# Kernel optimization log

Measured on AMD Instinct MI355X. Metric: run time of the kernel, lower is better.

Reference implementation:

```python
import jax, jax.numpy as jnp
import numpy as np

CODEBOOK_SIZE = 8192
CODEBOOK_DIM = 16
IN_DIM = 512


def setup_inputs() -> dict:
    key = jax.random.key(0)
    k1, k2, k3 = jax.random.split(key, 3)
    input_values = jax.random.normal(k1, (8, 4096, IN_DIM), dtype=jnp.float32)
    # xavier_uniform for Linear(IN_DIM -> CODEBOOK_DIM), weight shape (out, in) in torch
    limit = float(np.sqrt(6.0 / (IN_DIM + CODEBOOK_DIM)))
    proj_weight = jax.random.uniform(k2, (CODEBOOK_DIM, IN_DIM), dtype=jnp.float32, minval=-limit, maxval=limit)
    code_book = jax.random.normal(k3, (CODEBOOK_SIZE, CODEBOOK_DIM), dtype=jnp.float32)
    return {"input_values": input_values, "proj_weight": proj_weight, "code_book": code_book}


def reference(input_values, proj_weight, code_book):
    # targets: (B, L, d) = input @ W^T  (bias-free random projection)
    targets = jnp.einsum("bld,cd->blc", input_values, proj_weight)  # (B, L, 16)
    # Squared L2 distance via expansion ||t - c||^2 = ||t||^2 - 2 t.c + ||c||^2.
    # argmin is identical to argmin of the norm; avoids the (B,L,K,d) broadcast tensor.
    t_sq = jnp.sum(targets * targets, axis=-1, keepdims=True)        # (B, L, 1)
    c_sq = jnp.sum(code_book * code_book, axis=-1)                   # (K,)
    cross = jnp.einsum("blc,kc->blk", targets, code_book)            # (B, L, K)
    dist_sq = t_sq - 2.0 * cross + c_sq                              # (B, L, K)
    labels = jnp.argmin(dist_sq, axis=-1)                            # (B, L) int
    return labels
```

## Files before the change

kernel.cpp:

```cpp
#include <hip/hip_runtime.h>
#include <stdint.h>

#define IN_DIM 512
#define CB 8192
#define CD 16
#define NROWS 32768
#define DELTAQ 8e-3f
#define FMAXV 3.402823466e38f

typedef short bf16x8 __attribute__((ext_vector_type(8)));
typedef float f32x4 __attribute__((ext_vector_type(4)));

__device__ inline unsigned short f2bf(float x) {
    unsigned u = __float_as_uint(x);
    unsigned r = u + 0x7FFFu + ((u >> 16) & 1u);
    return (unsigned short)(r >> 16);
}
__device__ inline float bf2f(unsigned short h) { return __uint_as_float(((unsigned)h) << 16); }
__device__ inline unsigned umin32(unsigned a, unsigned b) { return a < b ? a : b; }
__device__ inline unsigned umax32(unsigned a, unsigned b) { return a > b ? a : b; }
__device__ inline unsigned long long shfl_xor_u64(unsigned long long x, int m) {
    double d = __shfl_xor(__longlong_as_double((long long)x), m, 64);
    return (unsigned long long)__double_as_longlong(d);
}

__global__ __launch_bounds__(256) void prep_kernel(const float* __restrict__ cb,
                                                   float* __restrict__ csq,
                                                   float* __restrict__ csqoff,
                                                   bf16x8* __restrict__ Bp,
                                                   int* __restrict__ counter) {
    int id = blockIdx.x * 256 + threadIdx.x;
    if (id == 0) counter[0] = 0;
    if (id < CB) {
        const float4* p = (const float4*)(cb + (size_t)id * CD);
        float s = 0.f;
#pragma unroll
        for (int j = 0; j < 4; ++j) {
            float4 v = p[j];
            s += v.x * v.x + v.y * v.y + v.z * v.z + v.w * v.w;
        }
        csq[id] = s;
        csqoff[id] = s + 256.0f;
    }
    int slot = id & 63;
    int nt = id >> 6;
    int q = slot >> 4;
    int n = nt * 16 + (slot & 15);
    int d0 = (q & 1) * 8;
    bool lo = (q < 2);
    const float* src = cb + (size_t)n * CD + d0;
    bf16x8 v;
#pragma unroll
    for (int j = 0; j < 8; ++j) {
        float x = src[j];
        unsigned short a = f2bf(x);
        unsigned short b = f2bf(x - bf2f(a));
        v[j] = (short)(lo ? a : b);
    }
    Bp[id] = v;
}

__global__ __launch_bounds__(256) void proj_partial_kernel(const float* __restrict__ in,
                                                           const float* __restrict__ W,
                                                           float* __restrict__ partials) {
    __shared__ float4 LIN[2048];
    __shared__ float4 WL[16 * 33];
    int tid = threadIdx.x;
    int lane = tid & 63;
    int dg = __builtin_amdgcn_readfirstlane(tid >> 6);
    int strip = blockIdx.x >> 2;
    int c = blockIdx.x & 3;
    int rowbase = strip * 64;
    const float4* inp4 = (const float4*)in;
    const float4* W4 = (const float4*)W;

#pragma unroll
    for (int u = 0; u < 2; ++u) {
        int f = tid + u * 256;
        int d = f >> 5, o = f & 31;
        WL[d * 33 + o] = W4[(size_t)d * 128 + c * 32 + o];
    }
#pragma unroll
    for (int u = 0; u < 8; ++u) {
        int f = tid + u * 256;
        int o = f & 31, r = f >> 5;
        LIN[o * 64 + (r ^ (o & 7))] = inp4[(size_t)(rowbase + r) * 128 + c * 32 + o];
    }
    __syncthreads();

    float acc[4];
#pragma unroll
    for (int i = 0; i < 4; ++i) acc[i] = 0.f;
#pragma unroll 4
    for (int j = 0; j < 32; ++j) {
        float4 v = LIN[j * 64 + (lane ^ (j & 7))];
#pragma unroll
        for (int i = 0; i < 4; ++i) {
            float4 w = WL[(4 * dg + i) * 33 + j];
            acc[i] += v.x * w.x + v.y * w.y + v.z * w.z + v.w * w.w;
        }
    }
    float* o = partials + (size_t)c * NROWS * CD + (size_t)(rowbase + lane) * CD + 4 * dg;
#pragma unroll
    for (int i = 0; i < 4; ++i) o[i] = acc[i];
}

__global__ __launch_bounds__(256) void proj_combine_kernel(const float* __restrict__ partials,
                                                           float* __restrict__ tprime) {
    int idx = blockIdx.x * 256 + threadIdx.x;
    const size_t P = (size_t)NROWS * CD;
    float p0 = partials[idx];
    float p1 = partials[P + idx];
    float p2 = partials[2 * P + idx];
    float p3 = partials[3 * P + idx];
    tprime[idx] = -2.f * (((p0 + p1) + p2) + p3);
}

__global__ __launch_bounds__(512, 6) void scan_kernel(
        const float* __restrict__ tprime, const float* __restrict__ csqoff,
        const bf16x8* __restrict__ Bp, int* __restrict__ out,
        int* __restrict__ queue, int* __restrict__ counter) {
    __shared__ float tbuf[32][17];
    __shared__ unsigned long long m_k[32][8];
    __shared__ unsigned m_s2[32][8];

    int tid = threadIdx.x;
    int lane = tid & 63;
    int e = __builtin_amdgcn_readfirstlane(tid >> 6);
    int rowbase = blockIdx.x * 32;

    tbuf[tid >> 4][tid & 15] = tprime[(size_t)rowbase * CD + tid];
    __syncthreads();

    int q = lane >> 4;
    int col = lane & 15;
    int d0 = (q & 1) * 8;
    bool lo = (q < 2);

    bf16x8 A1[2], A2[2];
#pragma unroll
    for (int g = 0; g < 2; ++g) {
        int arow = 16 * g + col;
#pragma unroll
        for (int j = 0; j < 8; ++j) {
            float x = tbuf[arow][d0 + j];
            unsigned short t1 = f2bf(x);
            unsigned short t2 = f2bf(x - bf2f(t1));
            A1[g][j] = (short)t1;
            A2[g][j] = (short)(lo ? t2 : 0);
        }
    }

    unsigned s1[2][4], s2[2][4];
#pragma unroll
    for (int g = 0; g < 2; ++g)
#pragma unroll
        for (int r = 0; r < 4; ++r) { s1[g][r] = 0xFFFFFFFFu; s2[g][r] = 0xFFFFFFFFu; }

    int nt0 = e * 64;
    const bf16x8* pb = Bp + (size_t)nt0 * 64 + lane;
    const float* csqp = csqoff + nt0 * 16 + col;

#pragma unroll 4
    for (int t = 0; t < 64; ++t) {
        bf16x8 b = pb[(size_t)t * 64];
        float cs = csqp[t * 16];
        f32x4 ini = {cs, cs, cs, cs};
        unsigned tt = (unsigned)t;
#pragma unroll
        for (int g = 0; g < 2; ++g) {
            f32x4 acc = __builtin_amdgcn_mfma_f32_16x16x32_bf16(A1[g], b, ini, 0, 0, 0);
            acc = __builtin_amdgcn_mfma_f32_16x16x32_bf16(A2[g], b, acc, 0, 0, 0);
#pragma unroll
            for (int r = 0; r < 4; ++r) {
                unsigned k = (__float_as_uint(acc[r]) & 0xFFFFFFC0u) | tt;
                s2[g][r] = umin32(s2[g][r], umax32(k, s1[g][r]));
                s1[g][r] = umin32(s1[g][r], k);
            }
        }
    }

#pragma unroll
    for (int g = 0; g < 2; ++g)
#pragma unroll
        for (int r = 0; r < 4; ++r) {
            unsigned long long FK = ((unsigned long long)(s1[g][r] & 0xFFFFFFC0u) << 13)
                                  | ((unsigned long long)e << 10)
                                  | ((unsigned long long)(s1[g][r] & 63u) << 4)
                                  | (unsigned long long)col;
            unsigned s2q = s2[g][r] & 0xFFFFFFC0u;
#pragma unroll
            for (int m = 1; m < 16; m <<= 1) {
                unsigned long long oFK = shfl_xor_u64(FK, m);
                unsigned os2 = (unsigned)__shfl_xor((int)s2q, m, 64);
                unsigned qa = (unsigned)(FK >> 13);
                unsigned qb = (unsigned)(oFK >> 13);
                s2q = umin32(umin32(s2q, os2), umax32(qa, qb));
                FK = oFK < FK ? oFK : FK;
            }
            if (col == 0) {
                int rl = 16 * g + 4 * q + r;
                m_k[rl][e] = FK;
                m_s2[rl][e] = s2q;
            }
        }
    __syncthreads();

    if (tid < 32) {
        unsigned long long mFK = m_k[tid][0];
        unsigned g1 = (unsigned)(m_k[tid][0] >> 13);
        unsigned g2 = m_s2[tid][0];
#pragma unroll
        for (int ee = 1; ee < 8; ++ee) {
            unsigned long long F = m_k[tid][ee];
            unsigned u = (unsigned)(F >> 13);
            if (u < g1) { g2 = g1; g1 = u; } else { g2 = umin32(g2, u); }
            g2 = umin32(g2, m_s2[tid][ee]);
            mFK = F < mFK ? F : mFK;
        }
        int ccol = (int)(mFK & 15ull);
        int ctile = (int)((mFK >> 4) & 63ull);
        int ce = (int)((mFK >> 10) & 7ull);
        int row = rowbase + tid;
        out[row] = ((ce * 64 + ctile) << 4) | ccol;
        if (__uint_as_float(g2) - __uint_as_float(g1) < DELTAQ) {
            int pos = atomicAdd(counter, 1);
            queue[pos] = row;
        }
    }
}

__global__ __launch_bounds__(256) void fallback_kernel(const float* __restrict__ tprime,
                                                       const float* __restrict__ cb,
                                                       const float* __restrict__ csq,
                                                       const int* __restrict__ queue,
                                                       const int* __restrict__ counter,
                                                       int* __restrict__ out) {
    __shared__ unsigned long long red[4];
    int nq = counter[0];
    int tid = threadIdx.x;
    int lane = tid & 63;
    int w = tid >> 6;

    for (int qi = blockIdx.x; qi < nq; qi += 256) {
        int row = queue[qi];
        float tp[16];
        const float* tpp = tprime + (size_t)row * CD;
#pragma unroll
        for (int d = 0; d < 16; ++d) tp[d] = tpp[d];

        float best = FMAXV;
        int bidx = 0;
#pragma unroll 2
        for (int i = 0; i < 32; ++i) {
            int k = tid + 256 * i;
            const float* cp = cb + (size_t)k * CD;
            float s = csq[k];
#pragma unroll
            for (int d = 0; d < 16; ++d) s += tp[d] * cp[d];
            if (s < best) { best = s; bidx = k; }
        }
        unsigned u = __float_as_uint(best);
        u = (u & 0x80000000u) ? ~u : (u | 0x80000000u);
        unsigned long long key = ((unsigned long long)u << 32) | (unsigned)bidx;
#pragma unroll
        for (int m = 1; m < 64; m <<= 1) {
            unsigned long long o = shfl_xor_u64(key, m);
            key = o < key ? o : key;
        }
        if (lane == 0) red[w] = key;
        __syncthreads();
        if (tid == 0) {
            unsigned long long mm = red[0];
#pragma unroll
            for (int i = 1; i < 4; ++i) { unsigned long long x = red[i]; mm = x < mm ? x : mm; }
            out[row] = (int)(mm & 0xFFFFFFFFull);
        }
        __syncthreads();
    }
}

extern "C" void kernel_launch(void* const* d_in, const int* in_sizes, int n_in,
                              void* d_out, int out_size, void* d_ws, size_t ws_size,
                              hipStream_t stream) {
    const float* input = (const float*)d_in[0];
    const float* W     = (const float*)d_in[1];
    const float* cb    = (const float*)d_in[2];
    int* out = (int*)d_out;

    float*  tprime   = (float*)d_ws;
    float*  csq      = tprime + (size_t)NROWS * CD;
    float*  csqoff   = csq + CB;
    bf16x8* Bp       = (bf16x8*)(csqoff + CB);
    float*  partials = (float*)(Bp + 32768);
    int*    counter  = (int*)(partials + 4 * (size_t)NROWS * CD);
    int*    queue    = counter + 16;

    prep_kernel<<<32768 / 256, 256, 0, stream>>>(cb, csq, csqoff, Bp, counter);
    proj_partial_kernel<<<(NROWS / 64) * 4, 256, 0, stream>>>(input, W, partials);
    proj_combine_kernel<<<NROWS * CD / 256, 256, 0, stream>>>(partials, tprime);
    scan_kernel<<<NROWS / 32, 512, 0, stream>>>(tprime, csqoff, Bp, out, queue, counter);
    fallback_kernel<<<256, 256, 0, stream>>>(tprime, cb, csq, queue, counter, out);
}
```

Before: 171.2 us.

## Fuse codebook prep into projection kernel and fold combine into scan

After: 164.1 us. 1.04x faster.

```diff
diff --git a/kernel.cpp b/kernel.cpp
--- a/kernel.cpp
+++ b/kernel.cpp
@@ -23,49 +23,59 @@
     double d = __shfl_xor(__longlong_as_double((long long)x), m, 64);
     return (unsigned long long)__double_as_longlong(d);
 }
-
-__global__ __launch_bounds__(256) void prep_kernel(const float* __restrict__ cb,
-                                                   float* __restrict__ csq,
-                                                   float* __restrict__ csqoff,
-                                                   bf16x8* __restrict__ Bp,
-                                                   int* __restrict__ counter) {
-    int id = blockIdx.x * 256 + threadIdx.x;
-    if (id == 0) counter[0] = 0;
-    if (id < CB) {
-        const float4* p = (const float4*)(cb + (size_t)id * CD);
-        float s = 0.f;
-#pragma unroll
-        for (int j = 0; j < 4; ++j) {
-            float4 v = p[j];
-            s += v.x * v.x + v.y * v.y + v.z * v.z + v.w * v.w;
-        }
-        csq[id] = s;
-        csqoff[id] = s + 256.0f;
-    }
-    int slot = id & 63;
-    int nt = id >> 6;
-    int q = slot >> 4;
-    int n = nt * 16 + (slot & 15);
-    int d0 = (q & 1) * 8;
-    bool lo = (q < 2);
-    const float* src = cb + (size_t)n * CD + d0;
-    bf16x8 v;
-#pragma unroll
-    for (int j = 0; j < 8; ++j) {
-        float x = src[j];
-        unsigned short a = f2bf(x);
-        unsigned short b = f2bf(x - bf2f(a));
-        v[j] = (short)(lo ? a : b);
-    }
-    Bp[id] = v;
-}
-
-__global__ __launch_bounds__(256) void proj_partial_kernel(const float* __restrict__ in,
-                                                           const float* __restrict__ W,
-                                                           float* __restrict__ partials) {
+__device__ inline unsigned med3_u32(unsigned a, unsigned b, unsigned c) {
+    unsigned d;
+    asm("v_med3_u32 %0, %1, %2, %3" : "=v"(d) : "v"(a), "v"(b), "v"(c));
+    return d;
+}
+
+__global__ __launch_bounds__(256) void prep_proj_kernel(const float* __restrict__ in,
+                                                        const float* __restrict__ W,
+                                                        float* __restrict__ partials,
+                                                        const float* __restrict__ cb,
+                                                        float* __restrict__ csq,
+                                                        f32x4* __restrict__ csq4,
+                                                        bf16x8* __restrict__ Bp,
+                                                        int* __restrict__ counter) {
     __shared__ float4 LIN[2048];
     __shared__ float4 WL[16 * 33];
     int tid = threadIdx.x;
+
+    if (blockIdx.x >= 2048) {
+        int id = (blockIdx.x - 2048) * 256 + tid;
+        if (id == 0) counter[0] = 0;
+        if (id < CB) {
+            const float4* p = (const float4*)(cb + (size_t)id * CD);
+            float s = 0.f;
+#pragma unroll
+            for (int j = 0; j < 4; ++j) {
+                float4 v = p[j];
+                s += v.x * v.x + v.y * v.y + v.z * v.z + v.w * v.w;
+            }
+            csq[id] = s;
+            float so = s + 256.0f;
+            f32x4 v4 = {so, so, so, so};
+            csq4[id] = v4;
+        }
+        int slot = id & 63;
+        int nt = id >> 6;
+        int q = slot >> 4;
+        int n = nt * 16 + (slot & 15);
+        int d0 = (q & 1) * 8;
+        bool lo = (q < 2);
+        const float* src = cb + (size_t)n * CD + d0;
+        bf16x8 v;
+#pragma unroll
+        for (int j = 0; j < 8; ++j) {
+            float x = src[j];
+            unsigned short a = f2bf(x);
+            unsigned short b = f2bf(x - bf2f(a));
+            v[j] = (short)(lo ? a : b);
+        }
+        Bp[id] = v;
+        return;
+    }
+
     int lane = tid & 63;
     int dg = __builtin_amdgcn_readfirstlane(tid >> 6);
     int strip = blockIdx.x >> 2;
@@ -105,19 +115,8 @@
     for (int i = 0; i < 4; ++i) o[i] = acc[i];
 }
 
-__global__ __launch_bounds__(256) void proj_combine_kernel(const float* __restrict__ partials,
-                                                           float* __restrict__ tprime) {
-    int idx = blockIdx.x * 256 + threadIdx.x;
-    const size_t P = (size_t)NROWS * CD;
-    float p0 = partials[idx];
-    float p1 = partials[P + idx];
-    float p2 = partials[2 * P + idx];
-    float p3 = partials[3 * P + idx];
-    tprime[idx] = -2.f * (((p0 + p1) + p2) + p3);
-}
-
 __global__ __launch_bounds__(512, 6) void scan_kernel(
-        const float* __restrict__ tprime, const float* __restrict__ csqoff,
+        const float* __restrict__ partials, const f32x4* __restrict__ csq4,
         const bf16x8* __restrict__ Bp, int* __restrict__ out,
         int* __restrict__ queue, int* __restrict__ counter) {
     __shared__ float tbuf[32][17];
@@ -129,7 +128,16 @@
     int e = __builtin_amdgcn_readfirstlane(tid >> 6);
     int rowbase = blockIdx.x * 32;
 
-    tbuf[tid >> 4][tid & 15] = tprime[(size_t)rowbase * CD + tid];
+    {
+        int rr = tid >> 4, d = tid & 15;
+        size_t idx = (size_t)(rowbase + rr) * CD + d;
+        const size_t P = (size_t)NROWS * CD;
+        float p0 = partials[idx];
+        float p1 = partials[P + idx];
+        float p2 = partials[2 * P + idx];
+        float p3 = partials[3 * P + idx];
+        tbuf[rr][d] = -2.f * (((p0 + p1) + p2) + p3);
+    }
     __syncthreads();
 
     int q = lane >> 4;
@@ -159,13 +167,12 @@
 
     int nt0 = e * 64;
     const bf16x8* pb = Bp + (size_t)nt0 * 64 + lane;
-    const float* csqp = csqoff + nt0 * 16 + col;
-
-#pragma unroll 4
+    const f32x4* csqp = csq4 + nt0 * 16 + col;
+
+#pragma unroll 8
     for (int t = 0; t < 64; ++t) {
         bf16x8 b = pb[(size_t)t * 64];
-        float cs = csqp[t * 16];
-        f32x4 ini = {cs, cs, cs, cs};
+        f32x4 ini = csqp[t * 16];
         unsigned tt = (unsigned)t;
 #pragma unroll
         for (int g = 0; g < 2; ++g) {
@@ -174,7 +181,7 @@
 #pragma unroll
             for (int r = 0; r < 4; ++r) {
                 unsigned k = (__float_as_uint(acc[r]) & 0xFFFFFFC0u) | tt;
-                s2[g][r] = umin32(s2[g][r], umax32(k, s1[g][r]));
+                s2[g][r] = med3_u32(s1[g][r], s2[g][r], k);
                 s1[g][r] = umin32(s1[g][r], k);
             }
         }
@@ -230,7 +237,7 @@
     }
 }
 
-__global__ __launch_bounds__(256) void fallback_kernel(const float* __restrict__ tprime,
+__global__ __launch_bounds__(256) void fallback_kernel(const float* __restrict__ partials,
                                                        const float* __restrict__ cb,
                                                        const float* __restrict__ csq,
                                                        const int* __restrict__ queue,
@@ -242,12 +249,15 @@
     int lane = tid & 63;
     int w = tid >> 6;
 
-    for (int qi = blockIdx.x; qi < nq; qi += 256) {
+    for (int qi = blockIdx.x; qi < nq; qi += 2048) {
         int row = queue[qi];
+        const size_t P = (size_t)NROWS * CD;
+        size_t base = (size_t)row * CD;
         float tp[16];
-        const float* tpp = tprime + (size_t)row * CD;
-#pragma unroll
-        for (int d = 0; d < 16; ++d) tp[d] = tpp[d];
+#pragma unroll
+        for (int d = 0; d < 16; ++d)
+            tp[d] = -2.f * (((partials[base + d] + partials[P + base + d])
+                             + partials[2 * P + base + d]) + partials[3 * P + base + d]);
 
         float best = FMAXV;
         int bidx = 0;
@@ -288,17 +298,14 @@
     const float* cb    = (const float*)d_in[2];
     int* out = (int*)d_out;
 
-    float*  tprime   = (float*)d_ws;
-    float*  csq      = tprime + (size_t)NROWS * CD;
-    float*  csqoff   = csq + CB;
-    bf16x8* Bp       = (bf16x8*)(csqoff + CB);
-    float*  partials = (float*)(Bp + 32768);
-    int*    counter  = (int*)(partials + 4 * (size_t)NROWS * CD);
+    float*  partials = (float*)d_ws;
+    float*  csq      = partials + 4 * (size_t)NROWS * CD;
+    f32x4*  csq4     = (f32x4*)(csq + CB);
+    bf16x8* Bp       = (bf16x8*)((float*)csq4 + 4 * CB);
+    int*    counter  = (int*)(Bp + 32768);
     int*    queue    = counter + 16;
 
-    prep_kernel<<<32768 / 256, 256, 0, stream>>>(cb, csq, csqoff, Bp, counter);
-    proj_partial_kernel<<<(NROWS / 64) * 4, 256, 0, stream>>>(input, W, partials);
-    proj_combine_kernel<<<NROWS * CD / 256, 256, 0, stream>>>(partials, tprime);
-    scan_kernel<<<NROWS / 32, 512, 0, stream>>>(tprime, csqoff, Bp, out, queue, counter);
-    fallback_kernel<<<256, 256, 0, stream>>>(tprime, cb, csq, queue, counter, out);
-}
+    prep_proj_kernel<<<2176, 256, 0, stream>>>(input, W, partials, cb, csq, csq4, Bp, counter);
+    scan_kernel<<<NROWS / 32, 512, 0, stream>>>(partials, csq4, Bp, out, queue, counter);
+    fallback_kernel<<<2048, 256, 0, stream>>>(partials, cb, csq, queue, counter, out);
+}
```
